# Performance work log

Hardware: AMD Instinct MI355X
Metric: run time of the kernel (lower is better)

Reference implementation:

```python
import jax, jax.numpy as jnp
import numpy as np

B, T, C, H, E, MIN_EXPERTS = 4, 2048, 2048, 128, 16, 2
ROPE_BASE = 10000.0


def setup_inputs() -> dict:
    key = jax.random.key(0)
    ks = jax.random.split(key, 6)
    hidden_states = jax.random.normal(ks[0], (B, T, C), jnp.float32)
    position_ids = jnp.arange(T, dtype=jnp.int32)[None, :]  # [1, T]
    sim_matrix = jax.random.normal(ks[1], (C, E), jnp.float32)
    gates = jnp.zeros((E,), jnp.float32)
    s_in = float(np.sqrt(6.0 / (C + H)))   # xavier_uniform bound for (C,H)
    s_out = float(np.sqrt(6.0 / (H + C)))
    q_proj = jax.random.uniform(ks[2], (E, C, H), jnp.float32, -s_in, s_in)
    k_proj = jax.random.uniform(ks[3], (E, C, H), jnp.float32, -s_in, s_in)
    v_proj = jax.random.uniform(ks[4], (E, C, H), jnp.float32, -s_in, s_in)
    o_proj = jax.random.uniform(ks[5], (E, H, C), jnp.float32, -s_out, s_out)
    return dict(hidden_states=hidden_states, position_ids=position_ids,
                sim_matrix=sim_matrix, gates=gates,
                q_proj=q_proj, k_proj=k_proj, v_proj=v_proj, o_proj=o_proj)


def _rotate_half(x):
    h = x.shape[-1] // 2
    return jnp.concatenate([-x[..., h:], x[..., :h]], axis=-1)


def _apply_rope(q, k, position_ids, seq_len, dim, dtype):
    inv_freq = 1.0 / (ROPE_BASE ** (jnp.arange(0, dim, 2, dtype=jnp.float32) / dim))
    t = jnp.arange(seq_len, dtype=jnp.float32)
    freqs = jnp.outer(t, inv_freq)                       # [T, H/2]
    emb = jnp.concatenate([freqs, freqs], axis=-1)       # [T, H]
    cos = jnp.cos(emb).astype(dtype)[position_ids]       # [1, T, H] (broadcasts over batch)
    sin = jnp.sin(emb).astype(dtype)[position_ids]
    q_emb = q * cos + _rotate_half(q) * sin
    k_emb = k * cos + _rotate_half(k) * sin
    return q_emb, k_emb


def reference(hidden_states, position_ids, sim_matrix, gates, q_proj, k_proj, v_proj, o_proj):
    b, t, c = hidden_states.shape
    n = b * t
    h = q_proj.shape[-1]
    x = hidden_states.reshape(n, c)

    # ---- gating: normalize + matmul + sigmoid offset + relu + STE + topk fallback + masked softmax ----
    xn = x / jnp.clip(jnp.linalg.norm(x, axis=-1, keepdims=True), 1e-12)
    wn = sim_matrix / jnp.clip(jnp.linalg.norm(sim_matrix, axis=0, keepdims=True), 1e-12)
    logits = xn @ wn - jax.nn.sigmoid(gates)             # [N, E]
    gated = jax.nn.relu(logits)
    hard = (gated > 0).astype(x.dtype)                   # STE forward (hard 0/1 mask)
    inactive = jnp.sum(hard, axis=1) == 0                # [N]
    _, top_idx = jax.lax.top_k(logits, MIN_EXPERTS)      # [N, MIN]
    fb = jnp.zeros_like(hard).at[jnp.arange(n)[:, None], top_idx].set(1.0)
    mask = jnp.where(inactive[:, None], fb, hard)        # [N, E]
    masked_logits = jnp.where(mask > 0, gated, jnp.asarray(-1e9, gated.dtype))
    routing_weights = jax.nn.softmax(masked_logits, axis=-1)
    # torch only accumulates active (token, expert) pairs -> equivalent to weights * mask
    we = routing_weights * jax.lax.stop_gradient(mask)   # [N, E]

    # ---- per-expert QKV projections, weighted scatter-add (dense-equivalent grouped GEMM) ----
    q = jnp.einsum('ne,nc,ech->nh', we, x, q_proj).reshape(b, t, h)
    k = jnp.einsum('ne,nc,ech->nh', we, x, k_proj).reshape(b, t, h)
    v = jnp.einsum('ne,nc,ech->nh', we, x, v_proj).reshape(b, t, h)

    q, k = _apply_rope(q, k, position_ids, t, h, x.dtype)

    # ---- single-head causal attention ----
    scale = 1.0 / jnp.sqrt(jnp.asarray(h, x.dtype))
    scores = jnp.einsum('bqh,bkh->bqk', q, k) * scale    # [B, T, T]
    causal = jnp.tril(jnp.ones((t, t), bool))
    scores = jnp.where(causal, scores, jnp.finfo(x.dtype).min)
    attn = jnp.einsum('bqk,bkh->bqh', jax.nn.softmax(scores, axis=-1), v)

    # ---- per-expert output projection, weighted scatter-add ----
    attn_flat = attn.reshape(n, h)
    out = jnp.einsum('ne,nh,ehc->nc', we, attn_flat, o_proj).reshape(b, t, c)
    return out
```

## Files before the change

kernel.cpp:

```cpp
#include <hip/hip_runtime.h>
#include <hip/hip_fp16.h>

#define T_ 2048
#define C_ 2048
#define H_ 128
#define E_ 16
#define N_TOK 8192
#define NS_ 4
#define SCALE_ 0.08838834764831845f

typedef _Float16 f16;
typedef _Float16 f16x4 __attribute__((ext_vector_type(4)));
typedef _Float16 f16x8 __attribute__((ext_vector_type(8)));
typedef float f32x4 __attribute__((ext_vector_type(4)));
typedef unsigned int u32x4 __attribute__((ext_vector_type(4)));

#define MFMA(a,b,c) __builtin_amdgcn_mfma_f32_16x16x32_f16(a,b,c,0,0,0)

__device__ __forceinline__ void gload16(const void* g, void* l){
  __builtin_amdgcn_global_load_lds(
      (const __attribute__((address_space(1))) unsigned int*)g,
      (__attribute__((address_space(3))) unsigned int*)l, 16, 0, 0);
}

__global__ __launch_bounds__(256) void prep_kernel(const float* __restrict__ sim,
    const float* __restrict__ gates, double* __restrict__ wninv, double* __restrict__ sigg){
  __shared__ double part[16][17];
  int tid = threadIdx.x;
  int col = tid & 15, grp = tid >> 4;
  double ssq = 0.0;
  for (int r = grp; r < C_; r += 16){ float v = sim[r*E_ + col]; ssq += (double)v*(double)v; }
  part[grp][col] = ssq;
  __syncthreads();
  if (tid < E_){
    double s = 0.0;
    #pragma unroll
    for (int g2 = 0; g2 < 16; g2++) s += part[g2][tid];
    wninv[tid] = 1.0 / fmax(sqrt(s), 1e-12);
    sigg[tid]  = 1.0 / (1.0 + exp(-(double)gates[tid]));
  }
}

__global__ __launch_bounds__(256) void conv_x(const float* __restrict__ x, f16* __restrict__ xh){
  for (int v = blockIdx.x*256 + threadIdx.x; v < N_TOK*C_/4; v += 4096*256){
    f32x4 a = *(const f32x4*)&x[(size_t)v*4];
    f16x4 h; h[0]=(f16)a[0]; h[1]=(f16)a[1]; h[2]=(f16)a[2]; h[3]=(f16)a[3];
    *(f16x4*)&xh[(size_t)v*4] = h;
  }
}

__global__ __launch_bounds__(256) void conv_w(const float* __restrict__ qp,
    const float* __restrict__ kp, const float* __restrict__ vp, f16* __restrict__ wT){
  int ep = blockIdx.z; int e = ep/3, proj = ep - 3*e;
  const float* W = (proj==0?qp:(proj==1?kp:vp)) + (size_t)e*C_*H_;
  int k0 = blockIdx.x*64, j0 = blockIdx.y*64;
  __shared__ float t[64][65];
  int tid = threadIdx.x;
  #pragma unroll
  for (int i = 0; i < 4; i++){
    int s = tid + 256*i;
    int r = s >> 4, c4 = (s & 15)*4;
    f32x4 a = *(const f32x4*)&W[(size_t)(k0+r)*H_ + j0 + c4];
    t[r][c4]=a[0]; t[r][c4+1]=a[1]; t[r][c4+2]=a[2]; t[r][c4+3]=a[3];
  }
  __syncthreads();
  #pragma unroll
  for (int i = 0; i < 4; i++){
    int s = tid + 256*i;
    int jj = s >> 4, k4 = (s & 15)*4;
    f16x4 h;
    h[0]=(f16)t[k4][jj]; h[1]=(f16)t[k4+1][jj]; h[2]=(f16)t[k4+2][jj]; h[3]=(f16)t[k4+3][jj];
    *(f16x4*)&wT[((size_t)e*384 + proj*128 + j0 + jj)*C_ + k0 + k4] = h;
  }
}

__global__ __launch_bounds__(256) void conv_o(const float* __restrict__ op, f16* __restrict__ oT){
  int e = blockIdx.z;
  int n0 = blockIdx.x*64, k0 = blockIdx.y*64;
  __shared__ float t[64][65];
  int tid = threadIdx.x;
  #pragma unroll
  for (int i = 0; i < 4; i++){
    int s = tid + 256*i;
    int r = s >> 4, c4 = (s & 15)*4;
    f32x4 a = *(const f32x4*)&op[(size_t)e*H_*C_ + (size_t)(k0+r)*C_ + n0 + c4];
    t[r][c4]=a[0]; t[r][c4+1]=a[1]; t[r][c4+2]=a[2]; t[r][c4+3]=a[3];
  }
  __syncthreads();
  #pragma unroll
  for (int i = 0; i < 4; i++){
    int s = tid + 256*i;
    int nn = s >> 4, k4 = (s & 15)*4;
    f16x4 h;
    h[0]=(f16)t[k4][nn]; h[1]=(f16)t[k4+1][nn]; h[2]=(f16)t[k4+2][nn]; h[3]=(f16)t[k4+3][nn];
    *(f16x4*)&oT[((size_t)e*C_ + n0 + nn)*H_ + k0 + k4] = h;
  }
}

__global__ __launch_bounds__(256) void gate_kernel(const float* __restrict__ x,
    const float* __restrict__ sim, const double* __restrict__ wninv,
    const double* __restrict__ sigg, int* __restrict__ cnt,
    int* __restrict__ list, float* __restrict__ listw){
  __shared__ double dred[8][17];
  int tid = threadIdx.x;
  int wv = tid >> 6, l = tid & 63;
  int tok = l & 7, ko = l >> 3;
  int n0 = blockIdx.x * 8;
  const float* xr = x + (size_t)(n0 + tok) * C_;
  const float* sp = sim + wv*4;
  double accA[4] = {0,0,0,0}, accB[4] = {0,0,0,0};
  double ssqA = 0.0, ssqB = 0.0;
  int kbase = ko * 256;
  #pragma unroll 4
  for (int k = kbase; k < kbase + 256; k += 4){
    f32x4 xv = *(const f32x4*)&xr[k];
    #pragma unroll
    for (int j = 0; j < 4; j++){
      f32x4 sv = *(const f32x4*)&sp[(size_t)(k+j)*E_];
      double xd = (double)xv[j];
      if (j & 1){
        accB[0] += xd*(double)sv[0]; accB[1] += xd*(double)sv[1];
        accB[2] += xd*(double)sv[2]; accB[3] += xd*(double)sv[3];
        if (wv == 0) ssqB += xd*xd;
      } else {
        accA[0] += xd*(double)sv[0]; accA[1] += xd*(double)sv[1];
        accA[2] += xd*(double)sv[2]; accA[3] += xd*(double)sv[3];
        if (wv == 0) ssqA += xd*xd;
      }
    }
  }
  double acc[4];
  #pragma unroll
  for (int j = 0; j < 4; j++){
    acc[j] = accA[j] + accB[j];
    acc[j] += __shfl_xor(acc[j], 8);
    acc[j] += __shfl_xor(acc[j], 16);
    acc[j] += __shfl_xor(acc[j], 32);
  }
  double ssq = ssqA + ssqB;
  ssq += __shfl_xor(ssq, 8);
  ssq += __shfl_xor(ssq, 16);
  ssq += __shfl_xor(ssq, 32);
  if (l < 8){
    #pragma unroll
    for (int j = 0; j < 4; j++) dred[tok][wv*4 + j] = acc[j];
    if (wv == 0) dred[tok][16] = ssq;
  }
  __syncthreads();
  if (tid < 8){
    int n = n0 + tid;
    double inv = 1.0 / fmax(sqrt(dred[tid][16]), 1e-12);
    double logit[E_]; bool mask[E_]; int active = 0;
    #pragma unroll
    for (int e = 0; e < E_; e++){
      logit[e] = dred[tid][e] * inv * wninv[e] - sigg[e];
      mask[e] = logit[e] > 0.0;
      if (mask[e]) active++;
    }
    if (active == 0){
      int i1 = -1, i2 = -1; double b1 = -1e300, b2 = -1e300;
      for (int e = 0; e < E_; e++){
        double v = logit[e];
        if (v > b1){ b2 = b1; i2 = i1; b1 = v; i1 = e; }
        else if (v > b2){ b2 = v; i2 = e; }
      }
      mask[i1] = true; mask[i2] = true;
    }
    double mx = -1e300;
    for (int e = 0; e < E_; e++){ if (mask[e]) mx = fmax(mx, fmax(logit[e], 0.0)); }
    double ex[E_]; double sum = 0.0;
    for (int e = 0; e < E_; e++){
      double gval = fmax(logit[e], 0.0);
      ex[e] = mask[e] ? exp(gval - mx) : 0.0;
      sum += ex[e];
    }
    double isum = 1.0 / sum;
    for (int e = 0; e < E_; e++){
      if (mask[e]){
        int p = atomicAdd(&cnt[e], 1);
        list[e*N_TOK + p]  = n;
        listw[e*N_TOK + p] = (float)(ex[e]*isum);
      }
    }
  }
}

__global__ __launch_bounds__(64) void tile_builder(const int* __restrict__ cnt,
    int* __restrict__ tlist, int* __restrict__ ntile,
    int* __restrict__ tlist2, int* __restrict__ ntile2){
  __shared__ int nts[E_], nts2[E_];
  int tid = threadIdx.x;
  if (tid < E_){
    nts[tid]  = (cnt[tid] + 63) >> 6;
    nts2[tid] = (cnt[tid] + 127) >> 7;
  }
  __syncthreads();
  if (tid < E_){
    int base = 0, b2 = 0;
    for (int e = 0; e < tid; e++){ base += nts[e]; b2 += nts2[e]; }
    for (int t = 0; t < nts[tid];  t++) tlist[base + t] = (tid << 8) | t;
    for (int t = 0; t < nts2[tid]; t++) tlist2[b2 + t]  = (tid << 8) | t;
    if (tid == E_-1){ *ntile = base + nts[tid]; *ntile2 = b2 + nts2[tid]; }
  }
}

__global__ __launch_bounds__(256, 2) void qkv_gemm(const f16* __restrict__ xh,
    const f16* __restrict__ wT, const int* __restrict__ cnt,
    const int* __restrict__ list, const float* __restrict__ listw,
    const int* __restrict__ tlist2, const int* __restrict__ ntile2,
    float* __restrict__ qkv){
  __shared__ __align__(16) f16 a_s[2][128][64];
  __shared__ __align__(16) f16 b_s[2][128][64];
  __shared__ int tok_s[128];
  __shared__ float wgt_s[128];
  int nitems = (*ntile2) * 3;
  int tid = threadIdx.x;
  int l = tid & 63, wv = tid >> 6;
  int wm = wv >> 1, wn = wv & 1;
  int g = l >> 4, c = l & 15;
  for (int w = blockIdx.x; w < nitems; w += gridDim.x){
    int tile = w / 3, nb = w - tile*3;
    int ent = tlist2[tile];
    int e = ent >> 8, mt = ent & 255;
    int ce = cnt[e];
    int m0 = mt * 128;
    if (tid < 128){
      int gr = m0 + tid;
      tok_s[tid] = (gr < ce) ? list[e*N_TOK + gr] : 0;
      wgt_s[tid] = (gr < ce) ? listw[e*N_TOK + gr] : 0.f;
    }
    __syncthreads();
    const f16* Bbase = wT + ((size_t)e*384 + nb*128)*C_;
    const f16* agp[4]; const f16* bgp[4];
    #pragma unroll
    for (int i = 0; i < 4; i++){
      int id = tid + 256*i;
      int row = id >> 3, ch = id & 7;
      agp[i] = xh + (size_t)tok_s[row]*C_ + ch*8;
      bgp[i] = Bbase + (size_t)row*C_ + ch*8;
    }
    f32x4 acc[4][4];
    #pragma unroll
    for (int m = 0; m < 4; m++)
      #pragma unroll
      for (int n = 0; n < 4; n++) acc[m][n] = (f32x4){0.f,0.f,0.f,0.f};
    #pragma unroll
    for (int i = 0; i < 4; i++){
      int id = tid + 256*i;
      gload16(agp[i], &a_s[0][0][0] + (size_t)id*8);
      gload16(bgp[i], &b_s[0][0][0] + (size_t)id*8);
    }
    __syncthreads();
    int cur = 0;
    for (int k0 = 0; k0 < C_; k0 += 64){
      int nxt = k0 + 64;
      if (nxt < C_){
        int nb2 = cur ^ 1;
        #pragma unroll
        for (int i = 0; i < 4; i++){
          int id = tid + 256*i;
          gload16(agp[i] + nxt, &a_s[nb2][0][0] + (size_t)id*8);
          gload16(bgp[i] + nxt, &b_s[nb2][0][0] + (size_t)id*8);
        }
      }
      #pragma unroll
      for (int ks = 0; ks < 2; ks++){
        f16x8 af[4], bf[4];
        #pragma unroll
        for (int m = 0; m < 4; m++)
          af[m] = *(const f16x8*)&a_s[cur][wm*64 + m*16 + c][ks*32 + 8*g];
        #pragma unroll
        for (int n = 0; n < 4; n++)
          bf[n] = *(const f16x8*)&b_s[cur][wn*64 + n*16 + c][ks*32 + 8*g];
        #pragma unroll
        for (int m = 0; m < 4; m++)
          #pragma unroll
          for (int n = 0; n < 4; n++)
            acc[m][n] = MFMA(af[m], bf[n], acc[m][n]);
      }
      __syncthreads();
      cur ^= 1;
    }
    #pragma unroll
    for (int m = 0; m < 4; m++){
      #pragma unroll
      for (int i = 0; i < 4; i++){
        int row = wm*64 + m*16 + 4*g + i;
        int gr = m0 + row;
        if (gr < ce){
          int tok = tok_s[row]; float wgt = wgt_s[row];
          #pragma unroll
          for (int n = 0; n < 4; n++){
            int col = nb*128 + wn*64 + n*16 + c;
            atomicAdd(&qkv[(size_t)tok*384 + col], wgt*acc[m][n][i]);
          }
        }
      }
    }
    __syncthreads();
  }
}

__global__ __launch_bounds__(192) void rope_kernel(const float* __restrict__ qkv,
    const int* __restrict__ pos_ids, f16* __restrict__ qh, f16* __restrict__ kh,
    f16* __restrict__ vh){
  int n = blockIdx.x; int tid = threadIdx.x;
  const float* row = qkv + (size_t)n * 384;
  if (tid < 128){
    int isK = tid >> 6, j = tid & 63;
    const float* src = row + isK*H_;
    float a = src[j], b = src[j+64];
    int pos = pos_ids[n & (T_-1)];
    float freq = exp2f(-(float)j * 0.20762050593046015f);
    float ang = (float)pos * freq;
    float s, cc;
    sincosf(ang, &s, &cc);
    f16* dst = isK ? kh : qh;
    dst[(size_t)n*H_ + j]      = (f16)(a*cc - b*s);
    dst[(size_t)n*H_ + j + 64] = (f16)(b*cc + a*s);
  } else {
    int j = (tid - 128)*2;
    vh[(size_t)n*H_ + j]     = (f16)row[256 + j];
    vh[(size_t)n*H_ + j + 1] = (f16)row[256 + j + 1];
  }
}

#define LDK_ 136
#define LDV_ 72
__global__ __launch_bounds__(128) void attn_kernel(const f16* __restrict__ qh,
    const f16* __restrict__ kh, const f16* __restrict__ vh,
    float* __restrict__ Opart, float* __restrict__ mlpart){
  int bid = blockIdx.x;
  int seg = blockIdx.y;
  int b = bid >> 6, qt = bid & 63;
  int q0 = qt*32, nbase = b*T_;
  __shared__ __align__(16) f16 q_s[32*LDK_];
  __shared__ __align__(16) f16 k_s[64*LDK_];
  __shared__ __align__(16) f16 v_s[128*LDV_];
  __shared__ __align__(16) f16 p_s[2*16*LDV_];
  int tid = threadIdx.x;
  int l = tid & 63, w = tid >> 6;
  int g = l >> 4, c = l & 15;
  #pragma unroll
  for (int i = 0; i < 4; i++){
    int slot = tid + 128*i;
    int ch = slot & 15, r = slot >> 4;
    *(u32x4*)&q_s[r*LDK_ + ch*8] = *(const u32x4*)&qh[((size_t)(nbase + q0 + r))*H_ + ch*8];
  }
  f32x4 oacc[8];
  #pragma unroll
  for (int nb = 0; nb < 8; nb++) oacc[nb] = (f32x4){0,0,0,0};
  float m_run[4], l_run[4];
  #pragma unroll
  for (int i = 0; i < 4; i++){ m_run[i] = -1e30f; l_run[i] = 0.f; }
  int nk = (q0 + 31)/64 + 1;
  for (int kt = seg; kt < nk; kt += NS_){
    int kb = kt*64;
    __syncthreads();
    #pragma unroll
    for (int i = 0; i < 8; i++){
      int slot = tid + 128*i;
      int ch = slot & 15, r = slot >> 4;
      *(u32x4*)&k_s[r*LDK_ + ch*8] = *(const u32x4*)&kh[((size_t)(nbase + kb + r))*H_ + ch*8];
    }
    #pragma unroll
    for (int i = 0; i < 8; i++){
      int slot = tid + 128*i;
      int tok = slot & 63, ch = slot >> 6;
      f16x8 raw = *(const f16x8*)&vh[((size_t)(nbase + kb + tok))*H_ + ch*8];
      #pragma unroll
      for (int j = 0; j < 8; j++) v_s[(ch*8 + j)*LDV_ + tok] = raw[j];
    }
    __syncthreads();
    f32x4 sacc[4];
    #pragma unroll
    for (int f = 0; f < 4; f++) sacc[f] = (f32x4){0,0,0,0};
    #pragma unroll
    for (int ks = 0; ks < 4; ks++){
      f16x8 qf = *(const f16x8*)&q_s[(w*16 + c)*LDK_ + ks*32 + 8*g];
      #pragma unroll
      for (int f = 0; f < 4; f++){
        f16x8 kf = *(const f16x8*)&k_s[(f*16 + c)*LDK_ + ks*32 + 8*g];
        sacc[f] = MFMA(qf, kf, sacc[f]);
      }
    }
    float tm[4];
    #pragma unroll
    for (int i = 0; i < 4; i++) tm[i] = -1e30f;
    #pragma unroll
    for (int f = 0; f < 4; f++){
      int kg = kb + f*16 + c;
      #pragma unroll
      for (int i = 0; i < 4; i++){
        int qg = q0 + w*16 + 4*g + i;
        float s = sacc[f][i] * SCALE_;
        if (kg > qg) s = -1e30f;
        sacc[f][i] = s;
        tm[i] = fmaxf(tm[i], s);
      }
    }
    #pragma unroll
    for (int i = 0; i < 4; i++){
      #pragma unroll
      for (int d = 1; d <= 8; d <<= 1) tm[i] = fmaxf(tm[i], __shfl_xor(tm[i], d));
      float mn = fmaxf(m_run[i], tm[i]);
      float al = __expf(m_run[i] - mn);
      m_run[i] = mn;
      l_run[i] *= al;
      #pragma unroll
      for (int nb = 0; nb < 8; nb++) oacc[nb][i] *= al;
    }
    float rs[4] = {0.f,0.f,0.f,0.f};
    #pragma unroll
    for (int f = 0; f < 4; f++){
      #pragma unroll
      for (int i = 0; i < 4; i++){
        float p = __expf(sacc[f][i] - m_run[i]);
        rs[i] += p;
        p_s[w*16*LDV_ + (4*g + i)*LDV_ + f*16 + c] = (f16)p;
      }
    }
    #pragma unroll
    for (int i = 0; i < 4; i++){
      #pragma unroll
      for (int d = 1; d <= 8; d <<= 1) rs[i] += __shfl_xor(rs[i], d);
      l_run[i] += rs[i];
    }
    #pragma unroll
    for (int ks = 0; ks < 2; ks++){
      f16x8 pf = *(const f16x8*)&p_s[w*16*LDV_ + c*LDV_ + ks*32 + 8*g];
      #pragma unroll
      for (int nb = 0; nb < 8; nb++){
        f16x8 vf = *(const f16x8*)&v_s[(c + 16*nb)*LDV_ + ks*32 + 8*g];
        oacc[nb] = MFMA(pf, vf, oacc[nb]);
      }
    }
  }
  #pragma unroll
  for (int i = 0; i < 4; i++){
    int row = w*16 + 4*g + i;
    size_t base = ((size_t)(seg*256 + bid)*32 + row);
    if (c == 0){
      mlpart[base*2]     = m_run[i];
      mlpart[base*2 + 1] = l_run[i];
    }
    float* orow = Opart + base*128;
    #pragma unroll
    for (int nb = 0; nb < 8; nb++)
      orow[c + 16*nb] = oacc[nb][i];
  }
}

__global__ __launch_bounds__(128) void attn_merge(const float* __restrict__ Opart,
    const float* __restrict__ mlpart, f16* __restrict__ ah){
  int bid = blockIdx.x;
  int tid = threadIdx.x;
  int row = tid & 31, d0 = (tid >> 5) * 32;
  float ms[NS_], lv[NS_], wgt[NS_];
  float m = -3e38f;
  #pragma unroll
  for (int s = 0; s < NS_; s++){
    size_t base = ((size_t)(s*256 + bid)*32 + row);
    ms[s] = mlpart[base*2];
    lv[s] = mlpart[base*2 + 1];
    m = fmaxf(m, ms[s]);
  }
  float wsum = 0.f;
  #pragma unroll
  for (int s = 0; s < NS_; s++){ wgt[s] = __expf(ms[s] - m); wsum += wgt[s]*lv[s]; }
  float inv = 1.f / wsum;
  int token = (bid >> 6)*T_ + (bid & 63)*32 + row;
  #pragma unroll
  for (int dd = 0; dd < 32; dd += 4){
    f32x4 o = (f32x4){0,0,0,0};
    #pragma unroll
    for (int s = 0; s < NS_; s++){
      f32x4 p = *(const f32x4*)&Opart[(((size_t)(s*256 + bid)*32 + row))*128 + d0 + dd];
      o[0] += wgt[s]*p[0]; o[1] += wgt[s]*p[1]; o[2] += wgt[s]*p[2]; o[3] += wgt[s]*p[3];
    }
    f16x4 h;
    h[0]=(f16)(o[0]*inv); h[1]=(f16)(o[1]*inv); h[2]=(f16)(o[2]*inv); h[3]=(f16)(o[3]*inv);
    *(f16x4*)&ah[(size_t)token*H_ + d0 + dd] = h;
  }
}

#define LDT 136
__global__ __launch_bounds__(256) void o_gemm(const f16* __restrict__ ah,
    const f16* __restrict__ oT, const int* __restrict__ cnt,
    const int* __restrict__ list, const float* __restrict__ listw,
    const int* __restrict__ tlist, const int* __restrict__ ntile,
    float* __restrict__ out){
  __shared__ __align__(16) f16 a_s[64*LDT];
  __shared__ __align__(16) f16 b_s[128*LDT];
  __shared__ int tok_s[64];
  __shared__ float wgt_s[64];
  int nitems = (*ntile) * 16;
  int tid = threadIdx.x;
  int l = tid & 63, wv = tid >> 6;
  int wm = wv >> 1, wn = wv & 1;
  int g = l >> 4, c = l & 15;
  for (int w = blockIdx.x; w < nitems; w += gridDim.x){
    int tile = w >> 4, nbt = w & 15;
    int ent = tlist[tile];
    int e = ent >> 8, mt = ent & 255;
    int ce = cnt[e];
    int m0 = mt * 64, n0 = nbt * 128;
    if (tid < 64){
      int gr = m0 + tid;
      tok_s[tid] = (gr < ce) ? list[e*N_TOK + gr] : 0;
      wgt_s[tid] = (gr < ce) ? listw[e*N_TOK + gr] : 0.f;
    }
    __syncthreads();
    #pragma unroll
    for (int i = 0; i < 4; i++){
      int s = tid + 256*i;
      int r = s >> 4, cs = (s & 15)*8;
      f16x8 v = *(const f16x8*)&ah[(size_t)tok_s[r]*H_ + cs];
      float wgt = wgt_s[r];
      f16x8 o;
      #pragma unroll
      for (int j = 0; j < 8; j++) o[j] = (f16)((float)v[j]*wgt);
      *(f16x8*)&a_s[r*LDT + cs] = o;
    }
    #pragma unroll
    for (int i = 0; i < 8; i++){
      int s = tid + 256*i;
      int j = s >> 4, cs = (s & 15)*8;
      f16x8 v = *(const f16x8*)&oT[((size_t)e*C_ + n0 + j)*H_ + cs];
      *(f16x8*)&b_s[j*LDT + cs] = v;
    }
    __syncthreads();
    f32x4 acc[2][4];
    #pragma unroll
    for (int m = 0; m < 2; m++)
      #pragma unroll
      for (int n = 0; n < 4; n++) acc[m][n] = (f32x4){0.f,0.f,0.f,0.f};
    #pragma unroll
    for (int ks = 0; ks < 4; ks++){
      f16x8 af[2], bf[4];
      #pragma unroll
      for (int m = 0; m < 2; m++)
        af[m] = *(const f16x8*)&a_s[(wm*32 + m*16 + c)*LDT + ks*32 + 8*g];
      #pragma unroll
      for (int n = 0; n < 4; n++)
        bf[n] = *(const f16x8*)&b_s[(wn*64 + n*16 + c)*LDT + ks*32 + 8*g];
      #pragma unroll
      for (int m = 0; m < 2; m++)
        #pragma unroll
        for (int n = 0; n < 4; n++)
          acc[m][n] = MFMA(af[m], bf[n], acc[m][n]);
    }
    #pragma unroll
    for (int m = 0; m < 2; m++){
      #pragma unroll
      for (int i = 0; i < 4; i++){
        int row = wm*32 + m*16 + 4*g + i;
        int gr = m0 + row;
        if (gr < ce){
          int tok = tok_s[row];
          #pragma unroll
          for (int n = 0; n < 4; n++){
            int col = n0 + wn*64 + n*16 + c;
            atomicAdd(&out[(size_t)tok*C_ + col], acc[m][n][i]);
          }
        }
      }
    }
    __syncthreads();
  }
}

extern "C" void kernel_launch(void* const* d_in, const int* in_sizes, int n_in,
                              void* d_out, int out_size, void* d_ws, size_t ws_size,
                              hipStream_t stream){
  const float* hs    = (const float*)d_in[0];
  const int*   pos   = (const int*)d_in[1];
  const float* sim   = (const float*)d_in[2];
  const float* gates = (const float*)d_in[3];
  const float* qp    = (const float*)d_in[4];
  const float* kp    = (const float*)d_in[5];
  const float* vp    = (const float*)d_in[6];
  const float* op    = (const float*)d_in[7];
  float* out = (float*)d_out;
  char* ws = (char*)d_ws;
  int*    cnt    = (int*)(ws + 0);
  int*    ntile  = (int*)(ws + 64);
  double* wninv  = (double*)(ws + 128);
  double* sigg   = (double*)(ws + 256);
  int*    tlist  = (int*)(ws + 512);
  int*    list   = (int*)(ws + 8704);
  float*  listw  = (float*)(ws + 532992);
  f16*    xh     = (f16*)(ws + 1057280);
  float*  Opart  = (float*)(ws + 1057280);
  float*  mlpart = (float*)(ws + 17834496);
  f16*    wT     = (f16*)(ws + 34611712);
  f16*    oT     = (f16*)(ws + 59777536);
  float*  qkv    = (float*)(ws + 68166144);
  f16*    ah     = (f16*)(ws + 68166144);
  f16*    qh     = (f16*)(ws + 80749056);
  f16*    kh     = (f16*)(ws + 82846208);
  f16*    vh     = (f16*)(ws + 84943360);
  int*    tlist2 = (int*)(ws + 87040512);
  int*    ntile2 = (int*)(ws + 87044608);

  hipMemsetAsync(cnt, 0, 64, stream);
  hipMemsetAsync(qkv, 0, (size_t)N_TOK*384*4, stream);
  hipMemsetAsync(out, 0, (size_t)N_TOK*C_*4, stream);

  prep_kernel<<<1, 256, 0, stream>>>(sim, gates, wninv, sigg);
  conv_x<<<4096, 256, 0, stream>>>(hs, xh);
  conv_w<<<dim3(32, 2, 48), 256, 0, stream>>>(qp, kp, vp, wT);
  conv_o<<<dim3(32, 2, 16), 256, 0, stream>>>(op, oT);
  gate_kernel<<<1024, 256, 0, stream>>>(hs, sim, wninv, sigg, cnt, list, listw);
  tile_builder<<<1, 64, 0, stream>>>(cnt, tlist, ntile, tlist2, ntile2);
  qkv_gemm<<<512, 256, 0, stream>>>(xh, wT, cnt, list, listw, tlist2, ntile2, qkv);
  rope_kernel<<<N_TOK, 192, 0, stream>>>(qkv, pos, qh, kh, vh);
  attn_kernel<<<dim3(256, NS_), 128, 0, stream>>>(qh, kh, vh, Opart, mlpart);
  attn_merge<<<256, 128, 0, stream>>>(Opart, mlpart, ah);
  o_gemm<<<2048, 256, 0, stream>>>(ah, oT, cnt, list, listw, tlist, ntile, out);
}
```

Before: 674.3 us.

## Split gating into LDS-staged split-K dot kernel and separate routing kernel

Gating is split in two. The dot-product kernel now stages the sim matrix in LDS and gives each block 32 tokens over one of four K segments, writing double partial sums to workspace. A second per-token kernel reduces the partials and does the routing and softmax with one thread per token, instead of 8 threads per 256-thread block. This should cut redundant global loads of sim and raise parallelism, at the cost of an extra launch and a workspace round-trip. The qkv memset moves after tile building because dpart aliases that buffer.

```diff
diff --git a/kernel.cpp b/kernel.cpp
--- a/kernel.cpp
+++ b/kernel.cpp
@@ -97,35 +97,42 @@
   }
 }
 
-__global__ __launch_bounds__(256) void gate_kernel(const float* __restrict__ x,
-    const float* __restrict__ sim, const double* __restrict__ wninv,
-    const double* __restrict__ sigg, int* __restrict__ cnt,
-    int* __restrict__ list, float* __restrict__ listw){
-  __shared__ double dred[8][17];
-  int tid = threadIdx.x;
-  int wv = tid >> 6, l = tid & 63;
-  int tok = l & 7, ko = l >> 3;
-  int n0 = blockIdx.x * 8;
+__global__ __launch_bounds__(256) void gate_dot(const float* __restrict__ x,
+    const float* __restrict__ sim, double* __restrict__ dpart){
+  __shared__ __align__(16) float st[4096];
+  int tid = threadIdx.x;
+  int eq = tid >> 6, l = tid & 63;
+  int tok = l & 31, kh = l >> 5;
+  int n0 = blockIdx.x * 32;
+  int seg = blockIdx.y;
   const float* xr = x + (size_t)(n0 + tok) * C_;
-  const float* sp = sim + wv*4;
   double accA[4] = {0,0,0,0}, accB[4] = {0,0,0,0};
   double ssqA = 0.0, ssqB = 0.0;
-  int kbase = ko * 256;
-  #pragma unroll 4
-  for (int k = kbase; k < kbase + 256; k += 4){
-    f32x4 xv = *(const f32x4*)&xr[k];
-    #pragma unroll
-    for (int j = 0; j < 4; j++){
-      f32x4 sv = *(const f32x4*)&sp[(size_t)(k+j)*E_];
-      double xd = (double)xv[j];
-      if (j & 1){
-        accB[0] += xd*(double)sv[0]; accB[1] += xd*(double)sv[1];
-        accB[2] += xd*(double)sv[2]; accB[3] += xd*(double)sv[3];
-        if (wv == 0) ssqB += xd*xd;
-      } else {
-        accA[0] += xd*(double)sv[0]; accA[1] += xd*(double)sv[1];
-        accA[2] += xd*(double)sv[2]; accA[3] += xd*(double)sv[3];
-        if (wv == 0) ssqA += xd*xd;
+  for (int k0 = seg*512; k0 < seg*512 + 512; k0 += 256){
+    __syncthreads();
+    #pragma unroll
+    for (int i = 0; i < 4; i++){
+      int idx = tid + 256*i;
+      *(f32x4*)&st[idx*4] = *(const f32x4*)&sim[(size_t)k0*E_ + idx*4];
+    }
+    __syncthreads();
+    #pragma unroll
+    for (int q = 0; q < 32; q++){
+      int kl = kh*128 + q*4;
+      f32x4 xv = *(const f32x4*)&xr[k0 + kl];
+      #pragma unroll
+      for (int j = 0; j < 4; j++){
+        f32x4 sv = *(const f32x4*)&st[(kl+j)*E_ + eq*4];
+        double xd = (double)xv[j];
+        if (j & 1){
+          accB[0] += xd*(double)sv[0]; accB[1] += xd*(double)sv[1];
+          accB[2] += xd*(double)sv[2]; accB[3] += xd*(double)sv[3];
+          if (eq == 0) ssqB += xd*xd;
+        } else {
+          accA[0] += xd*(double)sv[0]; accA[1] += xd*(double)sv[1];
+          accA[2] += xd*(double)sv[2]; accA[3] += xd*(double)sv[3];
+          if (eq == 0) ssqA += xd*xd;
+        }
       }
     }
   }
@@ -133,54 +140,61 @@
   #pragma unroll
   for (int j = 0; j < 4; j++){
     acc[j] = accA[j] + accB[j];
-    acc[j] += __shfl_xor(acc[j], 8);
-    acc[j] += __shfl_xor(acc[j], 16);
     acc[j] += __shfl_xor(acc[j], 32);
   }
   double ssq = ssqA + ssqB;
-  ssq += __shfl_xor(ssq, 8);
-  ssq += __shfl_xor(ssq, 16);
   ssq += __shfl_xor(ssq, 32);
-  if (l < 8){
-    #pragma unroll
-    for (int j = 0; j < 4; j++) dred[tok][wv*4 + j] = acc[j];
-    if (wv == 0) dred[tok][16] = ssq;
-  }
-  __syncthreads();
-  if (tid < 8){
-    int n = n0 + tid;
-    double inv = 1.0 / fmax(sqrt(dred[tid][16]), 1e-12);
-    double logit[E_]; bool mask[E_]; int active = 0;
-    #pragma unroll
+  if (l < 32){
+    double* dst = dpart + ((size_t)seg*N_TOK + n0 + tok)*17;
+    #pragma unroll
+    for (int j = 0; j < 4; j++) dst[eq*4 + j] = acc[j];
+    if (eq == 0) dst[16] = ssq;
+  }
+}
+
+__global__ __launch_bounds__(256) void gate_route(const double* __restrict__ dpart,
+    const double* __restrict__ wninv, const double* __restrict__ sigg,
+    int* __restrict__ cnt, int* __restrict__ list, float* __restrict__ listw){
+  int n = blockIdx.x*256 + threadIdx.x;
+  double v[17];
+  #pragma unroll
+  for (int j = 0; j < 17; j++) v[j] = 0.0;
+  for (int s = 0; s < NS_; s++){
+    const double* p = dpart + ((size_t)s*N_TOK + n)*17;
+    #pragma unroll
+    for (int j = 0; j < 17; j++) v[j] += p[j];
+  }
+  double inv = 1.0 / fmax(sqrt(v[16]), 1e-12);
+  double logit[E_]; bool mask[E_]; int active = 0;
+  #pragma unroll
+  for (int e = 0; e < E_; e++){
+    logit[e] = v[e] * inv * wninv[e] - sigg[e];
+    mask[e] = logit[e] > 0.0;
+    if (mask[e]) active++;
+  }
+  if (active == 0){
+    int i1 = -1, i2 = -1; double b1 = -1e300, b2 = -1e300;
     for (int e = 0; e < E_; e++){
-      logit[e] = dred[tid][e] * inv * wninv[e] - sigg[e];
-      mask[e] = logit[e] > 0.0;
-      if (mask[e]) active++;
-    }
-    if (active == 0){
-      int i1 = -1, i2 = -1; double b1 = -1e300, b2 = -1e300;
-      for (int e = 0; e < E_; e++){
-        double v = logit[e];
-        if (v > b1){ b2 = b1; i2 = i1; b1 = v; i1 = e; }
-        else if (v > b2){ b2 = v; i2 = e; }
-      }
-      mask[i1] = true; mask[i2] = true;
-    }
-    double mx = -1e300;
-    for (int e = 0; e < E_; e++){ if (mask[e]) mx = fmax(mx, fmax(logit[e], 0.0)); }
-    double ex[E_]; double sum = 0.0;
-    for (int e = 0; e < E_; e++){
-      double gval = fmax(logit[e], 0.0);
-      ex[e] = mask[e] ? exp(gval - mx) : 0.0;
-      sum += ex[e];
-    }
-    double isum = 1.0 / sum;
-    for (int e = 0; e < E_; e++){
-      if (mask[e]){
-        int p = atomicAdd(&cnt[e], 1);
-        list[e*N_TOK + p]  = n;
-        listw[e*N_TOK + p] = (float)(ex[e]*isum);
-      }
+      double vv = logit[e];
+      if (vv > b1){ b2 = b1; i2 = i1; b1 = vv; i1 = e; }
+      else if (vv > b2){ b2 = vv; i2 = e; }
+    }
+    mask[i1] = true; mask[i2] = true;
+  }
+  double mx = -1e300;
+  for (int e = 0; e < E_; e++){ if (mask[e]) mx = fmax(mx, fmax(logit[e], 0.0)); }
+  double ex[E_]; double sum = 0.0;
+  for (int e = 0; e < E_; e++){
+    double gval = fmax(logit[e], 0.0);
+    ex[e] = mask[e] ? exp(gval - mx) : 0.0;
+    sum += ex[e];
+  }
+  double isum = 1.0 / sum;
+  for (int e = 0; e < E_; e++){
+    if (mask[e]){
+      int p = atomicAdd(&cnt[e], 1);
+      list[e*N_TOK + p]  = n;
+      listw[e*N_TOK + p] = (float)(ex[e]*isum);
     }
   }
 }
@@ -596,6 +610,7 @@
   f16*    wT     = (f16*)(ws + 34611712);
   f16*    oT     = (f16*)(ws + 59777536);
   float*  qkv    = (float*)(ws + 68166144);
+  double* dpart  = (double*)(ws + 68166144);
   f16*    ah     = (f16*)(ws + 68166144);
   f16*    qh     = (f16*)(ws + 80749056);
   f16*    kh     = (f16*)(ws + 82846208);
@@ -604,15 +619,16 @@
   int*    ntile2 = (int*)(ws + 87044608);
 
   hipMemsetAsync(cnt, 0, 64, stream);
-  hipMemsetAsync(qkv, 0, (size_t)N_TOK*384*4, stream);
   hipMemsetAsync(out, 0, (size_t)N_TOK*C_*4, stream);
 
   prep_kernel<<<1, 256, 0, stream>>>(sim, gates, wninv, sigg);
   conv_x<<<4096, 256, 0, stream>>>(hs, xh);
   conv_w<<<dim3(32, 2, 48), 256, 0, stream>>>(qp, kp, vp, wT);
   conv_o<<<dim3(32, 2, 16), 256, 0, stream>>>(op, oT);
-  gate_kernel<<<1024, 256, 0, stream>>>(hs, sim, wninv, sigg, cnt, list, listw);
+  gate_dot<<<dim3(256, NS_), 256, 0, stream>>>(hs, sim, dpart);
+  gate_route<<<32, 256, 0, stream>>>(dpart, wninv, sigg, cnt, list, listw);
   tile_builder<<<1, 64, 0, stream>>>(cnt, tlist, ntile, tlist2, ntile2);
+  hipMemsetAsync(qkv, 0, (size_t)N_TOK*384*4, stream);
   qkv_gemm<<<512, 256, 0, stream>>>(xh, wT, cnt, list, listw, tlist2, ntile2, qkv);
   rope_kernel<<<N_TOK, 192, 0, stream>>>(qkv, pos, qh, kh, vh);
   attn_kernel<<<dim3(256, NS_), 128, 0, stream>>>(qh, kh, vh, Opart, mlpart);
```

Result: faster. 548.9 us (-18.6%).
